# Optimization experiments

Measured on AMD Instinct MI355X. Metric: run time of the kernel, lower is better.

## Reference

```python
import jax, jax.numpy as jnp
import numpy as np

B, S, E = 2, 2048, 1024
G, Q, D = 4, 4, 64          # n_groups, queries-per-group, head dim
SCALE = 1.0 / np.sqrt(E).astype(np.float32)  # sequence_attention=False -> 1/sqrt(embed_dim)


def setup_inputs() -> dict:
    key = jax.random.key(0)
    ks = jax.random.split(key, 12)
    init = lambda k, shp, fan_in: jax.random.uniform(k, shp, jnp.float32, -1.0, 1.0) / np.sqrt(fan_in)
    return {
        "q": jax.random.normal(ks[0], (B, S, E), jnp.float32),
        "k": jax.random.normal(ks[1], (B, S, E), jnp.float32),
        "v": jax.random.normal(ks[2], (B, S, E), jnp.float32),
        "Wq_w": init(ks[3], (E, G * Q * D), E),
        "Wq_b": init(ks[4], (G * Q * D,), E),
        "Wk_w": init(ks[5], (E, G * D), E),
        "Wk_b": init(ks[6], (G * D,), E),
        "Wv_w": init(ks[7], (E, G * D), E),
        "Wv_b": init(ks[8], (G * D,), E),
        "fc_w": init(ks[9], (G * Q * D, G * Q * D), G * Q * D),
        "fc_b": init(ks[10], (G * Q * D,), G * Q * D),
    }


def reference(q, k, v, Wq_w, Wq_b, Wk_w, Wk_b, Wv_w, Wv_b, fc_w, fc_b):
    # projections
    qh = (q @ Wq_w + Wq_b).reshape(B, S, G, Q, D)   # b s g q d
    kh = (k @ Wk_w + Wk_b).reshape(B, S, G, D)      # b s g d (1 KV head per group)
    vh = (v @ Wv_w + Wv_b).reshape(B, S, G, D)
    # energy: broadcast single KV head across Q query heads per group
    energy = jnp.einsum('bsgqd,btgd->bgqst', qh, kh) * SCALE  # [b,g,q,s,s]
    attn = jax.nn.softmax(energy, axis=-1)
    out = jnp.einsum('bgqst,btgd->bsgqd', attn, vh)           # b s g q d
    out = out.reshape(B, S, G * Q * D)                        # b s (g q d)
    return out @ fc_w + fc_b
```

## Files before the change

kernel.cpp:

```cpp
#include <hip/hip_runtime.h>


typedef unsigned short u16;
typedef __attribute__((ext_vector_type(4))) unsigned short u16x4;
typedef __attribute__((ext_vector_type(8))) short bf16x8;
typedef __attribute__((ext_vector_type(8))) unsigned short u16x8;
typedef __attribute__((ext_vector_type(4))) float f32x4;
typedef __attribute__((ext_vector_type(8))) float f32x8;

#define MFMA16(a, b, c) __builtin_amdgcn_mfma_f32_16x16x32_bf16(a, b, c, 0, 0, 0)

#define SC2L 0.045084140608f

__device__ __forceinline__ u16 f2b(float f) {
  unsigned int i = __builtin_bit_cast(unsigned int, f);
  i += 0x7fffu + ((i >> 16) & 1u);
  return (u16)(i >> 16);
}
__device__ __forceinline__ unsigned cvtpk_bf16(float a, float b) {
  unsigned r;
  asm("v_cvt_pk_bf16_f32 %0, %1, %2" : "=v"(r) : "v"(a), "v"(b));
  return r;
}
__device__ __forceinline__ void gload_lds16(const u16* g, u16* l) {
  __builtin_amdgcn_global_load_lds(
      (const __attribute__((address_space(1))) unsigned int*)g,
      (__attribute__((address_space(3))) unsigned int*)l, 16, 0, 0);
}

__global__ __launch_bounds__(256) void transpose_all(const float* __restrict__ Wq_w,
                                                     const float* __restrict__ Wk_w,
                                                     const float* __restrict__ Wv_w,
                                                     const float* __restrict__ fc_w,
                                                     u16* __restrict__ WqT,
                                                     u16* __restrict__ WkT,
                                                     u16* __restrict__ WvT,
                                                     u16* __restrict__ fcT) {
  __shared__ u16 tile[32][33];
  int r = blockIdx.x;
  const float* W; u16* Wt; int N; float scale;
  if (r < 1024)      { W = Wq_w; Wt = WqT; N = 1024; scale = SC2L; }
  else if (r < 1280) { W = Wk_w; Wt = WkT; N = 256;  scale = 1.0f; r -= 1024; }
  else if (r < 1536) { W = Wv_w; Wt = WvT; N = 256;  scale = 1.0f; r -= 1280; }
  else               { W = fc_w; Wt = fcT; N = 1024; scale = 1.0f; r -= 1536; }
  const int K = 1024;
  const int bk = (r & 31) * 32;
  const int bn = (r >> 5) * 32;
  const int tx = threadIdx.x & 31, ty = threadIdx.x >> 5;
#pragma unroll
  for (int rr = ty; rr < 32; rr += 8)
    tile[rr][tx] = f2b(W[(size_t)(bk + rr) * N + bn + tx] * scale);
  __syncthreads();
#pragma unroll
  for (int rr = ty; rr < 32; rr += 8) Wt[(size_t)(bn + rr) * K + bk + tx] = tile[tx][rr];
}

template <typename AT, typename CT>
__device__ __forceinline__ void gemm_body(const AT* __restrict__ A,
                                          const u16* __restrict__ Bt,
                                          const float* __restrict__ bias,
                                          CT* __restrict__ C,
                                          int M, int N, int K, float bscale,
                                          bool transv, int bid) {
  __shared__ alignas(16) u16 As[128 * 32];
  __shared__ alignas(16) u16 Bs[128 * 32];
  const int tid = threadIdx.x;
  const int lane = tid & 63, wave = tid >> 6;
  const int l15 = lane & 15, lg = lane >> 4;
  const int nb = N >> 7;
  const int bm = (bid / nb) << 7;
  const int bn = (bid % nb) << 7;
  const int wr = (wave >> 1) << 5;
  const int wc = (wave & 1) << 6;
  const int crow = tid >> 2;
  const int ccol = (tid & 3) * 8;

  f32x4 acc[2][4] = {};

  for (int k0 = 0; k0 < K; k0 += 32) {
    u16x8 av;
    if constexpr (__is_same(AT, float)) {
      const f32x8 af = *(const f32x8*)(A + (size_t)(bm + crow) * K + k0 + ccol);
      unsigned* aw = (unsigned*)&av;
#pragma unroll
      for (int j = 0; j < 4; ++j) aw[j] = cvtpk_bf16(af[2 * j], af[2 * j + 1]);
    }
    __syncthreads();
    if constexpr (__is_same(AT, float)) {
      *(u16x8*)(As + tid * 8) = av;
    } else {
      gload_lds16(A + (size_t)(bm + crow) * K + k0 + ccol, As + tid * 8);
    }
    gload_lds16(Bt + (size_t)(bn + crow) * K + k0 + ccol, Bs + tid * 8);
    __syncthreads();

    bf16x8 af[2], bf[4];
#pragma unroll
    for (int m = 0; m < 2; ++m)
      af[m] = *(const bf16x8*)(As + (wr + m * 16 + l15) * 32 + lg * 8);
#pragma unroll
    for (int n = 0; n < 4; ++n)
      bf[n] = *(const bf16x8*)(Bs + (wc + n * 16 + l15) * 32 + lg * 8);
#pragma unroll
    for (int m = 0; m < 2; ++m)
#pragma unroll
      for (int n = 0; n < 4; ++n) acc[m][n] = MFMA16(af[m], bf[n], acc[m][n]);
  }

  float bvv[4];
#pragma unroll
  for (int n = 0; n < 4; ++n) bvv[n] = bias[bn + wc + n * 16 + l15] * bscale;

  if (transv) {
#pragma unroll
    for (int m = 0; m < 2; ++m) {
      const int row = bm + wr + m * 16 + lg * 4;
      const int bb = row >> 11, t = row & 2047;
#pragma unroll
      for (int n = 0; n < 4; ++n) {
        const int col = bn + wc + n * 16 + l15;
        u16x4 pk;
#pragma unroll
        for (int rr = 0; rr < 4; ++rr) pk[rr] = f2b(acc[m][n][rr] + bvv[n]);
        *(u16x4*)(C + (size_t)bb * ((size_t)N * 2048) + (size_t)col * 2048 + t) = pk;
      }
    }
  } else {
#pragma unroll
    for (int m = 0; m < 2; ++m) {
      const int row = bm + wr + m * 16 + lg * 4;
#pragma unroll
      for (int rr = 0; rr < 4; ++rr) {
        CT* cp = C + (size_t)(row + rr) * N + bn + wc + l15;
#pragma unroll
        for (int n = 0; n < 4; ++n) {
          const float val = acc[m][n][rr] + bvv[n];
          if constexpr (__is_same(CT, u16)) cp[n * 16] = f2b(val);
          else                              cp[n * 16] = val;
        }
      }
    }
  }
}

__global__ __launch_bounds__(512) void gemm_qkv(const float* __restrict__ q,
                                                const float* __restrict__ k,
                                                const float* __restrict__ v,
                                                const u16* __restrict__ WqT,
                                                const u16* __restrict__ WkT,
                                                const u16* __restrict__ WvT,
                                                const float* __restrict__ Wq_b,
                                                const float* __restrict__ Wk_b,
                                                const float* __restrict__ Wv_b,
                                                u16* __restrict__ qh,
                                                u16* __restrict__ kh,
                                                u16* __restrict__ vt) {
  if (blockIdx.x < 256)
    gemm_body<float, u16>(q, WqT, Wq_b, qh, 4096, 1024, 1024, SC2L, false, blockIdx.x);
  else if (blockIdx.x < 320)
    gemm_body<float, u16>(k, WkT, Wk_b, kh, 4096, 256, 1024, 1.0f, false, blockIdx.x - 256);
  else
    gemm_body<float, u16>(v, WvT, Wv_b, vt, 4096, 256, 1024, 1.0f, true, blockIdx.x - 320);
}

template <typename AT, typename CT, bool TRANSV>
__global__ __launch_bounds__(512) void gemm_bt_bias(const AT* __restrict__ A,
                                                    const u16* __restrict__ Bt,
                                                    const float* __restrict__ bias,
                                                    CT* __restrict__ C,
                                                    int M, int N, int K, float bscale) {
  gemm_body<AT, CT>(A, Bt, bias, C, M, N, K, bscale, TRANSV, blockIdx.x);
}

__global__ __launch_bounds__(512, 2) void attn_fwd(const u16* __restrict__ qh,
                                                   const u16* __restrict__ kh,
                                                   const u16* __restrict__ vhT,
                                                   u16* __restrict__ ao) {
  constexpr int S = 2048;
  __shared__ alignas(16) u16 Klds[2][128][72];
  __shared__ alignas(16) u16 Vt[2][64][136];

  const int tid = threadIdx.x;
  const int lane = tid & 63, w = tid >> 6;
  const int h = w & 3, ssub = w >> 2;
  const int l15 = lane & 15, lg = lane >> 4;
  const int bid = blockIdx.x;
  const int s0 = (bid & 31) << 6;
  const int g = (bid >> 5) & 3;
  const int b = bid >> 7;
  const int sbase = s0 + ssub * 32;

  bf16x8 qf[2][2];
#pragma unroll
  for (int sh = 0; sh < 2; ++sh) {
    const u16* qrow = qh + (((size_t)(b * S + sbase + sh * 16 + l15)) << 10)
                      + g * 256 + h * 64 + lg * 8;
    qf[sh][0] = *(const bf16x8*)(qrow);
    qf[sh][1] = *(const bf16x8*)(qrow + 32);
  }

  const u16* kbase = kh + (((size_t)(b * S)) << 8) + g * 64;
  const u16* vtbase = vhT + ((size_t)(b * 256 + g * 64)) * 2048;

  float lsum[2] = {0.f, 0.f};
  f32x4 o[2][4] = {};

  const int srow = tid >> 3;
  const int sdp = (tid & 7) * 8;
  const int sig = (srow & 32) | (((srow >> 2) & 1) << 4) | (((srow >> 3) & 3) << 2) | (srow & 3);
  const int vrow = tid >> 4;
  const int vcol = (tid & 15) * 8;

  u16x8 kv[2], vv[2];
#define LOADTILE(T0)                                                                   \
  do {                                                                                 \
    kv[0] = *(const u16x8*)(kbase + (size_t)((T0) + srow) * 256 + sdp);                \
    kv[1] = *(const u16x8*)(kbase + (size_t)((T0) + 64 + srow) * 256 + sdp);           \
    vv[0] = *(const u16x8*)(vtbase + (size_t)vrow * 2048 + (T0) + vcol);               \
    vv[1] = *(const u16x8*)(vtbase + (size_t)(vrow + 32) * 2048 + (T0) + vcol);        \
  } while (0)

  LOADTILE(0);

#pragma unroll 2
  for (int i = 0; i < 16; ++i) {
    const int c = i & 1;
    *(u16x8*)(&Klds[c][sig][sdp])       = kv[0];
    *(u16x8*)(&Klds[c][sig + 64][sdp])  = kv[1];
    *(u16x8*)(&Vt[c][vrow][vcol])       = vv[0];
    *(u16x8*)(&Vt[c][vrow + 32][vcol])  = vv[1];
    __syncthreads();
    if (i + 1 < 16) LOADTILE((i + 1) << 7);

#pragma unroll
    for (int tt = 0; tt < 2; ++tt) {
#pragma unroll
      for (int kk = 0; kk < 2; ++kk) {
        float p[2][8];
#pragma unroll
        for (int nn = 0; nn < 2; ++nn) {
          const int n = kk * 2 + nn;
          const bf16x8 bk0 = *(const bf16x8*)(&Klds[c][tt * 64 + n * 16 + l15][lg * 8]);
          const bf16x8 bk1 = *(const bf16x8*)(&Klds[c][tt * 64 + n * 16 + l15][32 + lg * 8]);
          __builtin_amdgcn_s_setprio(1);
#pragma unroll
          for (int sh = 0; sh < 2; ++sh) {
            f32x4 z = {};
            z = MFMA16(bk0, qf[sh][0], z);
            z = MFMA16(bk1, qf[sh][1], z);
            __builtin_amdgcn_s_setprio(0);
#pragma unroll
            for (int r = 0; r < 4; ++r) {
              const float pv = exp2f(z[r]);
              lsum[sh] += pv;
              p[sh][nn * 4 + r] = pv;
            }
          }
        }
        bf16x8 pa[2];
#pragma unroll
        for (int sh = 0; sh < 2; ++sh) {
          unsigned* paw = (unsigned*)&pa[sh];
          paw[0] = cvtpk_bf16(p[sh][0], p[sh][1]);
          paw[1] = cvtpk_bf16(p[sh][2], p[sh][3]);
          paw[2] = cvtpk_bf16(p[sh][4], p[sh][5]);
          paw[3] = cvtpk_bf16(p[sh][6], p[sh][7]);
        }
        __builtin_amdgcn_s_setprio(1);
#pragma unroll
        for (int nd = 0; nd < 4; ++nd) {
          const bf16x8 bv = *(const bf16x8*)(&Vt[c][nd * 16 + l15][tt * 64 + kk * 32 + lg * 8]);
          o[0][nd] = MFMA16(pa[0], bv, o[0][nd]);
          o[1][nd] = MFMA16(pa[1], bv, o[1][nd]);
        }
        __builtin_amdgcn_s_setprio(0);
      }
    }
  }
#undef LOADTILE

#pragma unroll
  for (int sh = 0; sh < 2; ++sh) {
    float rs = lsum[sh];
    rs += __shfl_xor(rs, 16, 64);
    rs += __shfl_xor(rs, 32, 64);
    const float inv = 1.f / rs;
#pragma unroll
    for (int r = 0; r < 4; ++r) {
      const float invr = __shfl(inv, lg * 4 + r, 64);
      u16* orow = ao + (((size_t)(b * S + sbase + sh * 16 + lg * 4 + r)) << 10)
                  + g * 256 + h * 64 + l15;
#pragma unroll
      for (int nd = 0; nd < 4; ++nd) orow[nd * 16] = f2b(o[sh][nd][r] * invr);
    }
  }
}

extern "C" void kernel_launch(void* const* d_in, const int* in_sizes, int n_in,
                              void* d_out, int out_size, void* d_ws, size_t ws_size,
                              hipStream_t stream) {
  const float* q    = (const float*)d_in[0];
  const float* k    = (const float*)d_in[1];
  const float* v    = (const float*)d_in[2];
  const float* Wq_w = (const float*)d_in[3];
  const float* Wq_b = (const float*)d_in[4];
  const float* Wk_w = (const float*)d_in[5];
  const float* Wk_b = (const float*)d_in[6];
  const float* Wv_w = (const float*)d_in[7];
  const float* Wv_b = (const float*)d_in[8];
  const float* fc_w = (const float*)d_in[9];
  const float* fc_b = (const float*)d_in[10];
  float* out = (float*)d_out;

  u16* ws  = (u16*)d_ws;
  u16* WqT = ws;
  u16* WkT = WqT + 1024 * 1024;
  u16* WvT = WkT + 256 * 1024;
  u16* fcT = WvT + 256 * 1024;
  u16* qhp = fcT + 1024 * 1024;
  u16* khp = qhp + 4096 * 1024;
  u16* vtp = khp + 4096 * 256;
  u16* aop = vtp + 4096 * 256;

  transpose_all<<<2560, 256, 0, stream>>>(Wq_w, Wk_w, Wv_w, fc_w, WqT, WkT, WvT, fcT);

  gemm_qkv<<<384, 512, 0, stream>>>(q, k, v, WqT, WkT, WvT, Wq_b, Wk_b, Wv_b,
                                    qhp, khp, vtp);

  attn_fwd<<<256, 512, 0, stream>>>(qhp, khp, vtp, aop);

  gemm_bt_bias<u16, float, false><<<256, 512, 0, stream>>>(aop, fcT, fc_b, out, 4096, 1024, 1024, 1.0f);
}
```

Measured before the change: 118.5 us.

## Double-buffer GEMM LDS tiles to overlap global loads with MFMA

```diff
diff --git a/kernel.cpp b/kernel.cpp
--- a/kernel.cpp
+++ b/kernel.cpp
@@ -62,8 +62,8 @@
                                           CT* __restrict__ C,
                                           int M, int N, int K, float bscale,
                                           bool transv, int bid) {
-  __shared__ alignas(16) u16 As[128 * 32];
-  __shared__ alignas(16) u16 Bs[128 * 32];
+  __shared__ alignas(16) u16 As[2][128 * 32];
+  __shared__ alignas(16) u16 Bs[2][128 * 32];
   const int tid = threadIdx.x;
   const int lane = tid & 63, wave = tid >> 6;
   const int l15 = lane & 15, lg = lane >> 4;
@@ -74,37 +74,59 @@
   const int wc = (wave & 1) << 6;
   const int crow = tid >> 2;
   const int ccol = (tid & 3) * 8;
+  const AT*  arow = A  + (size_t)(bm + crow) * K + ccol;
+  const u16* brow = Bt + (size_t)(bn + crow) * K + ccol;
 
   f32x4 acc[2][4] = {};
-
-  for (int k0 = 0; k0 < K; k0 += 32) {
-    u16x8 av;
+  const int nt = K >> 5;
+
+  if constexpr (__is_same(AT, float)) {
+    const f32x8 af0 = *(const f32x8*)(arow);
+    u16x8 av; unsigned* aw = (unsigned*)&av;
+#pragma unroll
+    for (int j = 0; j < 4; ++j) aw[j] = cvtpk_bf16(af0[2 * j], af0[2 * j + 1]);
+    *(u16x8*)(As[0] + tid * 8) = av;
+  } else {
+    gload_lds16(arow, As[0] + tid * 8);
+  }
+  gload_lds16(brow, Bs[0] + tid * 8);
+  __syncthreads();
+
+#pragma unroll 2
+  for (int t = 0; t < nt; ++t) {
+    const int c = t & 1;
+    const int k1 = (t + 1) << 5;
+    f32x8 afn;
+    if (t + 1 < nt) {
+      if constexpr (__is_same(AT, float)) {
+        afn = *(const f32x8*)(arow + k1);
+      } else {
+        gload_lds16(arow + k1, As[c ^ 1] + tid * 8);
+      }
+      gload_lds16(brow + k1, Bs[c ^ 1] + tid * 8);
+    }
+
+    bf16x8 af[2], bf[4];
+#pragma unroll
+    for (int m = 0; m < 2; ++m)
+      af[m] = *(const bf16x8*)(As[c] + (wr + m * 16 + l15) * 32 + lg * 8);
+#pragma unroll
+    for (int n = 0; n < 4; ++n)
+      bf[n] = *(const bf16x8*)(Bs[c] + (wc + n * 16 + l15) * 32 + lg * 8);
+#pragma unroll
+    for (int m = 0; m < 2; ++m)
+#pragma unroll
+      for (int n = 0; n < 4; ++n) acc[m][n] = MFMA16(af[m], bf[n], acc[m][n]);
+
     if constexpr (__is_same(AT, float)) {
-      const f32x8 af = *(const f32x8*)(A + (size_t)(bm + crow) * K + k0 + ccol);
-      unsigned* aw = (unsigned*)&av;
-#pragma unroll
-      for (int j = 0; j < 4; ++j) aw[j] = cvtpk_bf16(af[2 * j], af[2 * j + 1]);
+      if (t + 1 < nt) {
+        u16x8 av; unsigned* aw = (unsigned*)&av;
+#pragma unroll
+        for (int j = 0; j < 4; ++j) aw[j] = cvtpk_bf16(afn[2 * j], afn[2 * j + 1]);
+        *(u16x8*)(As[c ^ 1] + tid * 8) = av;
+      }
     }
     __syncthreads();
-    if constexpr (__is_same(AT, float)) {
-      *(u16x8*)(As + tid * 8) = av;
-    } else {
-      gload_lds16(A + (size_t)(bm + crow) * K + k0 + ccol, As + tid * 8);
-    }
-    gload_lds16(Bt + (size_t)(bn + crow) * K + k0 + ccol, Bs + tid * 8);
-    __syncthreads();
-
-    bf16x8 af[2], bf[4];
-#pragma unroll
-    for (int m = 0; m < 2; ++m)
-      af[m] = *(const bf16x8*)(As + (wr + m * 16 + l15) * 32 + lg * 8);
-#pragma unroll
-    for (int n = 0; n < 4; ++n)
-      bf[n] = *(const bf16x8*)(Bs + (wc + n * 16 + l15) * 32 + lg * 8);
-#pragma unroll
-    for (int m = 0; m < 2; ++m)
-#pragma unroll
-      for (int n = 0; n < 4; ++n) acc[m][n] = MFMA16(af[m], bf[n], acc[m][n]);
   }
 
   float bvv[4];
```

After: 118.7 us. Within noise of the previous version (+0.2%).
